# Kernel tuning notes

Measured on AMD Instinct MI355X. Metric: run time of the kernel, lower is better.

The kernel has to match this reference:

```python
import jax, jax.numpy as jnp
import numpy as np

D_MODEL = 1024
NUM_HEADS = 16
HEAD_DIM = D_MODEL // NUM_HEADS
BATCH = 2
SEQ = 2048
POS_DIM = 64


def setup_inputs() -> dict:
    key = jax.random.key(0)
    ks = jax.random.split(key, 6)
    s = 1.0 / np.sqrt(D_MODEL)
    return {
        "x": jax.random.normal(ks[0], (BATCH, SEQ, D_MODEL), jnp.float32),
        "positions": jax.random.normal(ks[1], (SEQ, POS_DIM), jnp.float32),
        "Wq": jax.random.normal(ks[2], (D_MODEL, D_MODEL), jnp.float32) * s,
        "bq": jnp.zeros((D_MODEL,), jnp.float32),
        "Wk": jax.random.normal(ks[3], (D_MODEL, D_MODEL), jnp.float32) * s,
        "bk": jnp.zeros((D_MODEL,), jnp.float32),
        "Wv": jax.random.normal(ks[4], (D_MODEL, D_MODEL), jnp.float32) * s,
        "bv": jnp.zeros((D_MODEL,), jnp.float32),
        "Wo": jax.random.normal(ks[5], (D_MODEL, D_MODEL), jnp.float32) * s,
        "bo": jnp.zeros((D_MODEL,), jnp.float32),
    }


def _geodesic_distances(positions):
    # Euclidean manifold: log_map(p_i, p_j) = p_j - p_i, metric = Identity
    # -> d(i,j) = ||p_j - p_i||_2 ; diagonal is exactly 0 (matches i!=j skip).
    diff = positions[None, :, :] - positions[:, None, :]  # [S, S, P]
    return jnp.sqrt(jnp.sum(diff * diff, axis=-1))        # [S, S]


def reference(x, positions, Wq, bq, Wk, bk, Wv, bv, Wo, bo):
    B, S, _ = x.shape
    q = (x @ Wq + bq).reshape(B, S, NUM_HEADS, HEAD_DIM)
    k = (x @ Wk + bk).reshape(B, S, NUM_HEADS, HEAD_DIM)
    v = (x @ Wv + bv).reshape(B, S, NUM_HEADS, HEAD_DIM)
    distances = _geodesic_distances(positions)  # [S, S]
    scores = jnp.einsum('bihd,bjhd->bhij', q, k) / jnp.sqrt(
        jnp.asarray(HEAD_DIM, x.dtype))
    scores = scores - distances[None, None, :, :]
    weights = jax.nn.softmax(scores, axis=-1)
    out = jnp.einsum('bhij,bjhd->bihd', weights, v).reshape(B, S, D_MODEL)
    return out @ Wo + bo
```

## Files before the change

kernel.cpp:

```cpp
#include <hip/hip_runtime.h>
#include <hip/hip_bf16.h>

typedef __attribute__((ext_vector_type(8))) short short8;
typedef __attribute__((ext_vector_type(4))) float f32x4;

#define S_LEN 2048
#define DM 1024
#define NH 16
#define HD 64
#define PD 64

#define LOG2E 1.4426950408889634f

#if __has_builtin(__builtin_amdgcn_exp2f)
#define EXP2F(x) __builtin_amdgcn_exp2f(x)
#else
#define EXP2F(x) exp2f(x)
#endif

#define WAIT4_BARRIER() do {                                   \
    asm volatile("s_waitcnt vmcnt(4)" ::: "memory");           \
    __builtin_amdgcn_sched_barrier(0);                         \
    __builtin_amdgcn_s_barrier();                              \
  } while (0)

static __device__ inline float bf2f(unsigned short u) {
  union { unsigned int i; float f; } c;
  c.i = ((unsigned int)u) << 16;
  return c.f;
}
static __device__ inline unsigned short f2bf(float f) {
  __hip_bfloat16 h = __float2bfloat16(f);
  return *reinterpret_cast<unsigned short*>(&h);
}

static __device__ __forceinline__ void glds16(const void* g, void* l) {
  __builtin_amdgcn_global_load_lds(
      (__attribute__((address_space(1))) unsigned int*)(unsigned long long)g,
      (__attribute__((address_space(3))) unsigned int*)l, 16, 0, 0);
}


__global__ void convx_kernel(const float* __restrict__ x,
                             __hip_bfloat16* __restrict__ xb, int n4) {
  int i = blockIdx.x * blockDim.x + threadIdx.x;
  if (i >= n4) return;
  const float4 v = reinterpret_cast<const float4*>(x)[i];
  union { __hip_bfloat16 h[4]; ushort4 u; } o;
  o.h[0] = __float2bfloat16(v.x);
  o.h[1] = __float2bfloat16(v.y);
  o.h[2] = __float2bfloat16(v.z);
  o.h[3] = __float2bfloat16(v.w);
  reinterpret_cast<ushort4*>(xb)[i] = o.u;
}

__global__ void posprep_kernel(const float* __restrict__ pos,
                               __hip_bfloat16* __restrict__ posb,
                               float* __restrict__ pnorm) {
  int row = blockIdx.x, c = threadIdx.x;
  float v = pos[row * PD + c];
  posb[row * PD + c] = __float2bfloat16(v);
  float s = v * v;
#pragma unroll
  for (int m = 1; m < 64; m <<= 1) s += __shfl_xor(s, m);
  if (c == 0) pnorm[row] = s;
}

__global__ __launch_bounds__(256) void wtrans_kernel(
    const float* __restrict__ W0, const float* __restrict__ W1,
    const float* __restrict__ W2, const float* __restrict__ W3,
    __hip_bfloat16* __restrict__ T0, __hip_bfloat16* __restrict__ T1,
    __hip_bfloat16* __restrict__ T2, __hip_bfloat16* __restrict__ T3) {
  __shared__ float tile[32][33];
  const float* W = blockIdx.z == 0 ? W0 : blockIdx.z == 1 ? W1
                 : blockIdx.z == 2 ? W2 : W3;
  __hip_bfloat16* T = blockIdx.z == 0 ? T0 : blockIdx.z == 1 ? T1
                    : blockIdx.z == 2 ? T2 : T3;
  int tx = threadIdx.x & 31, ty = threadIdx.x >> 5;
  int k0 = blockIdx.x * 32, n0 = blockIdx.y * 32;
#pragma unroll
  for (int q = 0; q < 4; ++q)
    tile[ty + q * 8][tx] = W[(size_t)(k0 + ty + q * 8) * DM + n0 + tx];
  __syncthreads();
#pragma unroll
  for (int q = 0; q < 4; ++q)
    T[(size_t)(n0 + ty + q * 8) * DM + k0 + tx] =
        __float2bfloat16(tile[tx][ty + q * 8]);
}

__global__ __launch_bounds__(256) void dmt_kernel(
    const __hip_bfloat16* __restrict__ posb, const float* __restrict__ pnorm,
    __hip_bfloat16* __restrict__ dtout) {
  int tid = threadIdx.x;
  int lane = tid & 63, wid = tid >> 6;
  int lr = lane & 15, lh = lane >> 4;
  int wr = wid >> 1, wc = wid & 1;
  int m0 = blockIdx.x * 128 + wr * 64;
  int n0 = blockIdx.y * 64 + wc * 32;

  f32x4 acc[4][2];
#pragma unroll
  for (int mi = 0; mi < 4; ++mi)
#pragma unroll
    for (int ni = 0; ni < 2; ++ni) acc[mi][ni] = (f32x4){0.f, 0.f, 0.f, 0.f};

  const __hip_bfloat16* Ap = posb + (size_t)(m0 + lr) * PD + lh * 8;
  const __hip_bfloat16* Bp = posb + (size_t)(n0 + lr) * PD + lh * 8;

#pragma unroll
  for (int k0 = 0; k0 < PD; k0 += 32) {
    short8 a[4], b[2];
#pragma unroll
    for (int mi = 0; mi < 4; ++mi)
      a[mi] = *reinterpret_cast<const short8*>(Ap + (size_t)mi * 16 * PD + k0);
#pragma unroll
    for (int ni = 0; ni < 2; ++ni)
      b[ni] = *reinterpret_cast<const short8*>(Bp + (size_t)ni * 16 * PD + k0);
#pragma unroll
    for (int mi = 0; mi < 4; ++mi)
#pragma unroll
      for (int ni = 0; ni < 2; ++ni)
        acc[mi][ni] = __builtin_amdgcn_mfma_f32_16x16x32_bf16(
            a[mi], b[ni], acc[mi][ni], 0, 0, 0);
  }

#pragma unroll
  for (int mi = 0; mi < 4; ++mi) {
    float nim[4];
#pragma unroll
    for (int r = 0; r < 4; ++r) nim[r] = pnorm[m0 + mi * 16 + lh * 4 + r];
#pragma unroll
    for (int ni = 0; ni < 2; ++ni) {
      int j = n0 + ni * 16 + lr;
      float nj = pnorm[j];
      ushort4 o;
      unsigned short* op = &o.x;
#pragma unroll
      for (int r = 0; r < 4; ++r) {
        int i = m0 + mi * 16 + lh * 4 + r;
        float d2 = nim[r] + nj - 2.f * acc[mi][ni][r];
        float dist = (i == j) ? 0.f : sqrtf(fmaxf(d2, 0.f));
        op[r] = f2bf(-dist * LOG2E);
      }
      int qt = (m0 + mi * 16) >> 4;
      *reinterpret_cast<ushort4*>(dtout + ((size_t)qt * S_LEN + j) * 16 + lh * 4) = o;
    }
  }
}

__global__ __launch_bounds__(256) void gemm_qkv_kernel(
    const __hip_bfloat16* __restrict__ A, const __hip_bfloat16* __restrict__ Bt,
    const float* __restrict__ bq, const float* __restrict__ bk,
    const float* __restrict__ bv, __hip_bfloat16* __restrict__ qb,
    __hip_bfloat16* __restrict__ kb, __hip_bfloat16* __restrict__ vt) {
  const int K = DM;
  __shared__ __hip_bfloat16 abuf[2][4096];
  __shared__ __hip_bfloat16 bbuf[2][4096];
  int tid = threadIdx.x;
  int lane = tid & 63, w = tid >> 6;
  int lr = lane & 15, lh = lane >> 4;
  int wr = w >> 1, wc = w & 1;
  int m0 = blockIdx.x * 128;
  int n0 = blockIdx.y * 128;

  f32x4 acc[4][4];
#pragma unroll
  for (int mi = 0; mi < 4; ++mi)
#pragma unroll
    for (int ni = 0; ni < 4; ++ni) acc[mi][ni] = (f32x4){0.f, 0.f, 0.f, 0.f};

  const __hip_bfloat16* Ag = A + (size_t)(m0 + lr) * K + lh * 8;
  const __hip_bfloat16* Bg = Bt + (size_t)(n0 + lr) * K + lh * 8;

  auto STAGE = [&](int nb, int k0) {
#pragma unroll
    for (int q = 0; q < 2; ++q) {
      int g = w * 2 + q;
      glds16(Ag + (size_t)(g * 16) * K + k0, &abuf[nb][g * 512]);
      glds16(Bg + (size_t)(g * 16) * K + k0, &bbuf[nb][g * 512]);
    }
  };

  STAGE(0, 0);

  const int NT = K / 32;
  for (int t = 0; t < NT; ++t) {
    int cb = t & 1;
    STAGE(cb ^ 1, (t + 1 < NT) ? (t + 1) * 32 : 0);
    WAIT4_BARRIER();
    short8 a[4], b[4];
#pragma unroll
    for (int mi = 0; mi < 4; ++mi)
      a[mi] = *reinterpret_cast<const short8*>(&abuf[cb][(wr * 4 + mi) * 512 + lane * 8]);
#pragma unroll
    for (int ni = 0; ni < 4; ++ni)
      b[ni] = *reinterpret_cast<const short8*>(&bbuf[cb][(wc * 4 + ni) * 512 + lane * 8]);
#pragma unroll
    for (int mi = 0; mi < 4; ++mi)
#pragma unroll
      for (int ni = 0; ni < 4; ++ni)
        acc[mi][ni] = __builtin_amdgcn_mfma_f32_16x16x32_bf16(
            a[mi], b[ni], acc[mi][ni], 0, 0, 0);
    __builtin_amdgcn_s_barrier();
  }

#pragma unroll
  for (int mi = 0; mi < 4; ++mi)
#pragma unroll
    for (int ni = 0; ni < 4; ++ni)
#pragma unroll
      for (int r = 0; r < 4; ++r) {
        int row = m0 + wr * 64 + mi * 16 + lh * 4 + r;
        int col = n0 + wc * 64 + ni * 16 + lr;
        int which = col >> 10, within = col & 1023;
        int bb = row >> 11, s = row & 2047;
        int h = within >> 6, d = within & 63;
        const float* bias = which == 0 ? bq : which == 1 ? bk : bv;
        float v = acc[mi][ni][r] + bias[within];
        __hip_bfloat16 hv = __float2bfloat16(v);
        if (which == 0)
          qb[((size_t)(bb * NH + h) * S_LEN + s) * HD + d] = hv;
        else if (which == 1)
          kb[((size_t)(bb * NH + h) * S_LEN + s) * HD + d] = hv;
        else
          vt[((size_t)(bb * NH + h) * HD + d) * S_LEN + s] = hv;
      }
}

__global__ __launch_bounds__(256) void gemm_out_kernel(
    const __hip_bfloat16* __restrict__ A, const __hip_bfloat16* __restrict__ Bt,
    const float* __restrict__ bias, float* __restrict__ out) {
  const int K = DM, N = DM;
  int tid = threadIdx.x;
  int lane = tid & 63, wid = tid >> 6;
  int lr = lane & 15, lh = lane >> 4;
  int wr = wid >> 1, wc = wid & 1;
  int m0 = blockIdx.x * 128 + wr * 64;
  int n0 = blockIdx.y * 64 + wc * 32;

  f32x4 acc[4][2];
#pragma unroll
  for (int mi = 0; mi < 4; ++mi)
#pragma unroll
    for (int ni = 0; ni < 2; ++ni) acc[mi][ni] = (f32x4){0.f, 0.f, 0.f, 0.f};

  const __hip_bfloat16* Ap = A + (size_t)(m0 + lr) * K + lh * 8;
  const __hip_bfloat16* Bp = Bt + (size_t)(n0 + lr) * K + lh * 8;

  for (int k0 = 0; k0 < K; k0 += 32) {
    short8 a[4], b[2];
#pragma unroll
    for (int mi = 0; mi < 4; ++mi)
      a[mi] = *reinterpret_cast<const short8*>(Ap + (size_t)mi * 16 * K + k0);
#pragma unroll
    for (int ni = 0; ni < 2; ++ni)
      b[ni] = *reinterpret_cast<const short8*>(Bp + (size_t)ni * 16 * K + k0);
#pragma unroll
    for (int mi = 0; mi < 4; ++mi)
#pragma unroll
      for (int ni = 0; ni < 2; ++ni)
        acc[mi][ni] = __builtin_amdgcn_mfma_f32_16x16x32_bf16(
            a[mi], b[ni], acc[mi][ni], 0, 0, 0);
  }

#pragma unroll
  for (int mi = 0; mi < 4; ++mi)
#pragma unroll
    for (int ni = 0; ni < 2; ++ni)
#pragma unroll
      for (int r = 0; r < 4; ++r) {
        int row = m0 + mi * 16 + lh * 4 + r;
        int col = n0 + ni * 16 + lr;
        out[(size_t)row * N + col] = acc[mi][ni][r] + bias[col];
      }
}

__global__ __launch_bounds__(256) void attn_kernel(
    const __hip_bfloat16* __restrict__ qb, const __hip_bfloat16* __restrict__ kb,
    const __hip_bfloat16* __restrict__ vt, const __hip_bfloat16* __restrict__ dt,
    __hip_bfloat16* __restrict__ ob) {
  __shared__ __hip_bfloat16 kbuf[2][4096];
  __shared__ __hip_bfloat16 vbuf[2][4096];
  __shared__ __hip_bfloat16 plds[4][16 * 64];
  int tid = threadIdx.x;
  int lane = tid & 63, w = tid >> 6;
  int lr = lane & 15, lh = lane >> 4;
  int bh = blockIdx.y;
  int b = bh >> 4, h = bh & 15;
  int s0 = blockIdx.x * 64 + w * 16;
  int qt = s0 >> 4;

  const __hip_bfloat16* qh = qb + (size_t)bh * S_LEN * HD;
  const __hip_bfloat16* kh = kb + (size_t)bh * S_LEN * HD;
  const __hip_bfloat16* vh = vt + (size_t)bh * HD * S_LEN;

  short8 qf0 = *reinterpret_cast<const short8*>(qh + (size_t)(s0 + lr) * HD + lh * 8);
  short8 qf1 = *reinterpret_cast<const short8*>(qh + (size_t)(s0 + lr) * HD + 32 + lh * 8);

  f32x4 accO[4];
#pragma unroll
  for (int n = 0; n < 4; ++n) accO[n] = (f32x4){0.f, 0.f, 0.f, 0.f};
  f32x4 lacc = (f32x4){0.f, 0.f, 0.f, 0.f};

  short8 ones;
#pragma unroll
  for (int e = 0; e < 8; ++e) ones[e] = (short)0x3F80;

  const f32x4 z4 = (f32x4){0.f, 0.f, 0.f, 0.f};
  const float C2 = 0.125f * LOG2E;

  const __hip_bfloat16* kstg = kh + (size_t)(w * 16 + lr) * HD + lh * 8;
  const __hip_bfloat16* vstg = vh + (size_t)(w * 16 + lr) * S_LEN + lh * 8;
  const __hip_bfloat16* dtq = dt + ((size_t)qt * S_LEN + lr) * 16 + lh * 4;

  auto STAGE = [&](int nb, int j0n) {
#pragma unroll
    for (int kk = 0; kk < 2; ++kk)
      glds16(kstg + (size_t)j0n * HD + kk * 32, &kbuf[nb][(w * 2 + kk) * 512]);
#pragma unroll
    for (int jj = 0; jj < 2; ++jj)
      glds16(vstg + j0n + jj * 32, &vbuf[nb][(w * 2 + jj) * 512]);
  };

  STAGE(0, 0);

  const int NT = S_LEN / 64;
  for (int t = 0; t < NT; ++t) {
    int cb = t & 1;
    int j0 = t * 64;

    ushort4 dv[4];
#pragma unroll
    for (int jt = 0; jt < 4; ++jt)
      dv[jt] = *reinterpret_cast<const ushort4*>(dtq + (size_t)(j0 + jt * 16) * 16);

    STAGE(cb ^ 1, (t + 1 < NT) ? j0 + 64 : 0);
    WAIT4_BARRIER();

#pragma unroll
    for (int jt = 0; jt < 4; ++jt) {
      short8 kf0 = *reinterpret_cast<const short8*>(&kbuf[cb][(jt * 2 + 0) * 512 + lane * 8]);
      short8 kf1 = *reinterpret_cast<const short8*>(&kbuf[cb][(jt * 2 + 1) * 512 + lane * 8]);
      f32x4 s4 = __builtin_amdgcn_mfma_f32_16x16x32_bf16(qf0, kf0, z4, 0, 0, 0);
      s4 = __builtin_amdgcn_mfma_f32_16x16x32_bf16(qf1, kf1, s4, 0, 0, 0);
      const unsigned short* dp = &dv[jt].x;
#pragma unroll
      for (int r = 0; r < 4; ++r) {
        float score2 = s4[r] * C2 + bf2f(dp[r]);
        float p = EXP2F(score2);
        int row = lh * 4 + r;
        int c = jt * 16 + lr;
        int idx = row * 64 + (((c >> 3) ^ (row & 7)) << 3) + (c & 7);
        plds[w][idx] = __float2bfloat16(p);
      }
    }
#pragma unroll
    for (int p2 = 0; p2 < 2; ++p2) {
      short8 pfrag = *reinterpret_cast<const short8*>(
          &plds[w][lr * 64 + ((((p2 * 4 + lh)) ^ (lr & 7)) << 3)]);
      lacc = __builtin_amdgcn_mfma_f32_16x16x32_bf16(pfrag, ones, lacc, 0, 0, 0);
#pragma unroll
      for (int n = 0; n < 4; ++n) {
        short8 vf = *reinterpret_cast<const short8*>(
            &vbuf[cb][(n * 2 + p2) * 512 + lane * 8]);
        accO[n] = __builtin_amdgcn_mfma_f32_16x16x32_bf16(pfrag, vf, accO[n], 0, 0, 0);
      }
    }
    __builtin_amdgcn_s_barrier();
  }

  float inv[4];
#pragma unroll
  for (int r = 0; r < 4; ++r) inv[r] = 1.f / lacc[r];
#pragma unroll
  for (int n = 0; n < 4; ++n)
#pragma unroll
    for (int r = 0; r < 4; ++r) {
      int s = s0 + lh * 4 + r;
      ob[((size_t)(b * S_LEN) + s) * DM + h * HD + n * 16 + lr] =
          __float2bfloat16(accO[n][r] * inv[r]);
    }
}

extern "C" void kernel_launch(void* const* d_in, const int* in_sizes, int n_in,
                              void* d_out, int out_size, void* d_ws, size_t ws_size,
                              hipStream_t stream) {
  const float* x   = (const float*)d_in[0];
  const float* pos = (const float*)d_in[1];
  const float* Wq  = (const float*)d_in[2];
  const float* bq  = (const float*)d_in[3];
  const float* Wk  = (const float*)d_in[4];
  const float* bk  = (const float*)d_in[5];
  const float* Wv  = (const float*)d_in[6];
  const float* bv  = (const float*)d_in[7];
  const float* Wo  = (const float*)d_in[8];
  const float* bo  = (const float*)d_in[9];

  char* ws = (char*)d_ws;
  size_t off = 0;
  auto alloc = [&](size_t bytes) {
    char* p = ws + off;
    off += (bytes + 255) & ~(size_t)255;
    return p;
  };
  __hip_bfloat16* xb    = (__hip_bfloat16*)alloc((size_t)4096 * DM * 2);
  __hip_bfloat16* wqkvT = (__hip_bfloat16*)alloc((size_t)3 * DM * DM * 2);
  __hip_bfloat16* woT   = (__hip_bfloat16*)alloc((size_t)DM * DM * 2);
  __hip_bfloat16* posb  = (__hip_bfloat16*)alloc((size_t)S_LEN * PD * 2);
  float*          pnrm  = (float*)alloc((size_t)S_LEN * 4);
  __hip_bfloat16* qb    = (__hip_bfloat16*)alloc((size_t)2 * NH * S_LEN * HD * 2);
  __hip_bfloat16* kb    = (__hip_bfloat16*)alloc((size_t)2 * NH * S_LEN * HD * 2);
  __hip_bfloat16* vt    = (__hip_bfloat16*)alloc((size_t)2 * NH * S_LEN * HD * 2);
  __hip_bfloat16* ob    = (__hip_bfloat16*)alloc((size_t)4096 * DM * 2);
  __hip_bfloat16* dtb   = (__hip_bfloat16*)alloc((size_t)(S_LEN / 16) * S_LEN * 16 * 2);
  (void)ws_size;

  int n4 = 4096 * DM / 4;
  hipLaunchKernelGGL(convx_kernel, dim3((n4 + 255) / 256), dim3(256), 0, stream,
                     x, xb, n4);
  hipLaunchKernelGGL(posprep_kernel, dim3(S_LEN), dim3(64), 0, stream,
                     pos, posb, pnrm);
  hipLaunchKernelGGL(wtrans_kernel, dim3(32, 32, 4), dim3(256), 0, stream,
                     Wq, Wk, Wv, Wo,
                     wqkvT, wqkvT + (size_t)DM * DM, wqkvT + (size_t)2 * DM * DM, woT);

  hipLaunchKernelGGL(dmt_kernel, dim3(S_LEN / 128, S_LEN / 64), dim3(256), 0, stream,
                     posb, pnrm, dtb);

  hipLaunchKernelGGL(gemm_qkv_kernel, dim3(4096 / 128, 3072 / 128), dim3(256), 0,
                     stream, xb, wqkvT, bq, bk, bv, qb, kb, vt);

  hipLaunchKernelGGL(attn_kernel, dim3(S_LEN / 64, 2 * NH), dim3(256), 0, stream,
                     qb, kb, vt, dtb, ob);

  hipLaunchKernelGGL(gemm_out_kernel, dim3(4096 / 128, DM / 64), dim3(256), 0,
                     stream, ob, woT, bo, (float*)d_out);
}
```

Before: 294.3 us.

## Keep softmax probabilities in registers via transposed QK MFMA feeding 16x16x16 PV MFMA

Swaps the operand order of the QK^T MFMA so each lane holds four consecutive key columns for one query row. Those probabilities then pack directly into a 16x16x16 bf16 MFMA A-operand, removing the per-warp LDS round trip for P and the ones-vector MFMA used to form row sums. Row sums are now kept in a scalar and combined with lane shuffles. The distance matrix producer is changed to a plain row-major layout to match the new access pattern. In exchange, the PV product uses twice as many smaller MFMAs and reads V with narrower LDS loads.

Measured after the change: 341.1 us. 15.9% more time.

```diff
diff --git a/kernel.cpp b/kernel.cpp
--- a/kernel.cpp
+++ b/kernel.cpp
@@ -2,6 +2,7 @@
 #include <hip/hip_bf16.h>
 
 typedef __attribute__((ext_vector_type(8))) short short8;
+typedef __attribute__((ext_vector_type(4))) short s16x4;
 typedef __attribute__((ext_vector_type(4))) float f32x4;
 
 #define S_LEN 2048
@@ -16,6 +17,20 @@
 #define EXP2F(x) __builtin_amdgcn_exp2f(x)
 #else
 #define EXP2F(x) exp2f(x)
+#endif
+
+#if __has_builtin(__builtin_amdgcn_mfma_f32_16x16x16bf16_1k)
+#define MFMA16(a, b, c) __builtin_amdgcn_mfma_f32_16x16x16bf16_1k((a), (b), (c), 0, 0, 0)
+#elif __has_builtin(__builtin_amdgcn_mfma_f32_16x16x16_bf16)
+#define MFMA16(a, b, c) __builtin_amdgcn_mfma_f32_16x16x16_bf16((a), (b), (c), 0, 0, 0)
+#else
+static __device__ __forceinline__ f32x4 mfma16_asm(s16x4 a, s16x4 b, f32x4 c) {
+  f32x4 d;
+  asm volatile("v_mfma_f32_16x16x16_bf16 %0, %1, %2, %3"
+               : "=v"(d) : "v"(a), "v"(b), "v"(c));
+  return d;
+}
+#define MFMA16(a, b, c) mfma16_asm((a), (b), (c))
 #endif
 
 #define WAIT4_BARRIER() do {                                   \
@@ -121,29 +136,28 @@
 #pragma unroll
       for (int ni = 0; ni < 2; ++ni)
         acc[mi][ni] = __builtin_amdgcn_mfma_f32_16x16x32_bf16(
-            a[mi], b[ni], acc[mi][ni], 0, 0, 0);
+            b[ni], a[mi], acc[mi][ni], 0, 0, 0);
   }
 
 #pragma unroll
   for (int mi = 0; mi < 4; ++mi) {
-    float nim[4];
-#pragma unroll
-    for (int r = 0; r < 4; ++r) nim[r] = pnorm[m0 + mi * 16 + lh * 4 + r];
+    int i = m0 + mi * 16 + lr;
+    float ni_ = pnorm[i];
 #pragma unroll
     for (int ni = 0; ni < 2; ++ni) {
-      int j = n0 + ni * 16 + lr;
-      float nj = pnorm[j];
+      int jb = n0 + ni * 16 + lh * 4;
+      float4 njv = *reinterpret_cast<const float4*>(pnorm + jb);
+      const float* njp = &njv.x;
       ushort4 o;
       unsigned short* op = &o.x;
 #pragma unroll
       for (int r = 0; r < 4; ++r) {
-        int i = m0 + mi * 16 + lh * 4 + r;
-        float d2 = nim[r] + nj - 2.f * acc[mi][ni][r];
+        int j = jb + r;
+        float d2 = ni_ + njp[r] - 2.f * acc[mi][ni][r];
         float dist = (i == j) ? 0.f : sqrtf(fmaxf(d2, 0.f));
         op[r] = f2bf(-dist * LOG2E);
       }
-      int qt = (m0 + mi * 16) >> 4;
-      *reinterpret_cast<ushort4*>(dtout + ((size_t)qt * S_LEN + j) * 16 + lh * 4) = o;
+      *reinterpret_cast<ushort4*>(dtout + (size_t)i * S_LEN + jb) = o;
     }
   }
 }
@@ -281,14 +295,12 @@
     __hip_bfloat16* __restrict__ ob) {
   __shared__ __hip_bfloat16 kbuf[2][4096];
   __shared__ __hip_bfloat16 vbuf[2][4096];
-  __shared__ __hip_bfloat16 plds[4][16 * 64];
   int tid = threadIdx.x;
   int lane = tid & 63, w = tid >> 6;
   int lr = lane & 15, lh = lane >> 4;
   int bh = blockIdx.y;
   int b = bh >> 4, h = bh & 15;
   int s0 = blockIdx.x * 64 + w * 16;
-  int qt = s0 >> 4;
 
   const __hip_bfloat16* qh = qb + (size_t)bh * S_LEN * HD;
   const __hip_bfloat16* kh = kb + (size_t)bh * S_LEN * HD;
@@ -300,18 +312,14 @@
   f32x4 accO[4];
 #pragma unroll
   for (int n = 0; n < 4; ++n) accO[n] = (f32x4){0.f, 0.f, 0.f, 0.f};
-  f32x4 lacc = (f32x4){0.f, 0.f, 0.f, 0.f};
-
-  short8 ones;
-#pragma unroll
-  for (int e = 0; e < 8; ++e) ones[e] = (short)0x3F80;
+  float lsum = 0.f;
 
   const f32x4 z4 = (f32x4){0.f, 0.f, 0.f, 0.f};
   const float C2 = 0.125f * LOG2E;
 
   const __hip_bfloat16* kstg = kh + (size_t)(w * 16 + lr) * HD + lh * 8;
   const __hip_bfloat16* vstg = vh + (size_t)(w * 16 + lr) * S_LEN + lh * 8;
-  const __hip_bfloat16* dtq = dt + ((size_t)qt * S_LEN + lr) * 16 + lh * 4;
+  const __hip_bfloat16* dtq = dt + (size_t)(s0 + lr) * S_LEN + lh * 4;
 
   auto STAGE = [&](int nb, int j0n) {
 #pragma unroll
@@ -323,6 +331,7 @@
   };
 
   STAGE(0, 0);
+
 
   const int NT = S_LEN / 64;
   for (int t = 0; t < NT; ++t) {
@@ -332,7 +341,7 @@
     ushort4 dv[4];
 #pragma unroll
     for (int jt = 0; jt < 4; ++jt)
-      dv[jt] = *reinterpret_cast<const ushort4*>(dtq + (size_t)(j0 + jt * 16) * 16);
+      dv[jt] = *reinterpret_cast<const ushort4*>(dtq + j0 + jt * 16);
 
     STAGE(cb ^ 1, (t + 1 < NT) ? j0 + 64 : 0);
     WAIT4_BARRIER();
@@ -341,44 +350,43 @@
     for (int jt = 0; jt < 4; ++jt) {
       short8 kf0 = *reinterpret_cast<const short8*>(&kbuf[cb][(jt * 2 + 0) * 512 + lane * 8]);
       short8 kf1 = *reinterpret_cast<const short8*>(&kbuf[cb][(jt * 2 + 1) * 512 + lane * 8]);
-      f32x4 s4 = __builtin_amdgcn_mfma_f32_16x16x32_bf16(qf0, kf0, z4, 0, 0, 0);
-      s4 = __builtin_amdgcn_mfma_f32_16x16x32_bf16(qf1, kf1, s4, 0, 0, 0);
+      f32x4 s4 = __builtin_amdgcn_mfma_f32_16x16x32_bf16(kf0, qf0, z4, 0, 0, 0);
+      s4 = __builtin_amdgcn_mfma_f32_16x16x32_bf16(kf1, qf1, s4, 0, 0, 0);
       const unsigned short* dp = &dv[jt].x;
-#pragma unroll
-      for (int r = 0; r < 4; ++r) {
-        float score2 = s4[r] * C2 + bf2f(dp[r]);
-        float p = EXP2F(score2);
-        int row = lh * 4 + r;
-        int c = jt * 16 + lr;
-        int idx = row * 64 + (((c >> 3) ^ (row & 7)) << 3) + (c & 7);
-        plds[w][idx] = __float2bfloat16(p);
-      }
-    }
-#pragma unroll
-    for (int p2 = 0; p2 < 2; ++p2) {
-      short8 pfrag = *reinterpret_cast<const short8*>(
-          &plds[w][lr * 64 + ((((p2 * 4 + lh)) ^ (lr & 7)) << 3)]);
-      lacc = __builtin_amdgcn_mfma_f32_16x16x32_bf16(pfrag, ones, lacc, 0, 0, 0);
+      float p[4];
+#pragma unroll
+      for (int r = 0; r < 4; ++r)
+        p[r] = EXP2F(s4[r] * C2 + bf2f(dp[r]));
+      lsum += (p[0] + p[1]) + (p[2] + p[3]);
+      union { s16x4 v; __hip_bfloat162 h2[2]; } up;
+      up.h2[0] = __float22bfloat162_rn(make_float2(p[0], p[1]));
+      up.h2[1] = __float22bfloat162_rn(make_float2(p[2], p[3]));
+      s16x4 pa = up.v;
+      int j64 = jt * 16 + lh * 4;
+      int voff = ((j64 >> 5) * 512) + (((j64 & 31) >> 3) * 16 + lr) * 8 + (j64 & 7);
 #pragma unroll
       for (int n = 0; n < 4; ++n) {
-        short8 vf = *reinterpret_cast<const short8*>(
-            &vbuf[cb][(n * 2 + p2) * 512 + lane * 8]);
-        accO[n] = __builtin_amdgcn_mfma_f32_16x16x32_bf16(pfrag, vf, accO[n], 0, 0, 0);
+        s16x4 vf = *reinterpret_cast<const s16x4*>(&vbuf[cb][n * 1024 + voff]);
+        accO[n] = MFMA16(pa, vf, accO[n]);
       }
     }
     __builtin_amdgcn_s_barrier();
   }
 
-  float inv[4];
-#pragma unroll
-  for (int r = 0; r < 4; ++r) inv[r] = 1.f / lacc[r];
+  lsum += __shfl_xor(lsum, 16);
+  lsum += __shfl_xor(lsum, 32);
+  float inv_ = 1.f / lsum;
+  float invr[4];
+#pragma unroll
+  for (int r = 0; r < 4; ++r) invr[r] = __shfl(inv_, lh * 4 + r);
+
 #pragma unroll
   for (int n = 0; n < 4; ++n)
 #pragma unroll
     for (int r = 0; r < 4; ++r) {
       int s = s0 + lh * 4 + r;
       ob[((size_t)(b * S_LEN) + s) * DM + h * HD + n * 16 + lr] =
-          __float2bfloat16(accO[n][r] * inv[r]);
+          __float2bfloat16(accO[n][r] * invr[r]);
     }
 }
 
@@ -412,7 +420,7 @@
   __hip_bfloat16* kb    = (__hip_bfloat16*)alloc((size_t)2 * NH * S_LEN * HD * 2);
   __hip_bfloat16* vt    = (__hip_bfloat16*)alloc((size_t)2 * NH * S_LEN * HD * 2);
   __hip_bfloat16* ob    = (__hip_bfloat16*)alloc((size_t)4096 * DM * 2);
-  __hip_bfloat16* dtb   = (__hip_bfloat16*)alloc((size_t)(S_LEN / 16) * S_LEN * 16 * 2);
+  __hip_bfloat16* dtb   = (__hip_bfloat16*)alloc((size_t)S_LEN * S_LEN * 2);
   (void)ws_size;
 
   int n4 = 4096 * DM / 4;
```

## Split attention KV range across two wave groups per block and merge partials

Applied to the files above, without the earlier changes.

The attention kernel now launches 512 threads per block. Two groups of four waves each process half of the key/value sequence, with 32-key tiles staged into separate LDS regions. At the end, the second half writes its unnormalized output accumulators and row sums to LDS, and the first half adds them before normalizing. This raises the number of waves per query tile to improve latency hiding and MFMA utilization. In exchange it adds a final LDS reduction and barrier, halves the tile size (more barriers per key), and leaves only two waves per group staging K and V.

After: 309.2 us. 5.1% more time.

```diff
diff --git a/kernel.cpp b/kernel.cpp
--- a/kernel.cpp
+++ b/kernel.cpp
@@ -275,25 +275,30 @@
       }
 }
 
-__global__ __launch_bounds__(256) void attn_kernel(
+__global__ __launch_bounds__(512, 8) void attn_kernel(
     const __hip_bfloat16* __restrict__ qb, const __hip_bfloat16* __restrict__ kb,
     const __hip_bfloat16* __restrict__ vt, const __hip_bfloat16* __restrict__ dt,
     __hip_bfloat16* __restrict__ ob) {
-  __shared__ __hip_bfloat16 kbuf[2][4096];
-  __shared__ __hip_bfloat16 vbuf[2][4096];
-  __shared__ __hip_bfloat16 plds[4][16 * 64];
+  __shared__ __align__(16) char smem[40960];
   int tid = threadIdx.x;
   int lane = tid & 63, w = tid >> 6;
+  int wq = w & 3, half = w >> 2;
   int lr = lane & 15, lh = lane >> 4;
   int bh = blockIdx.y;
   int b = bh >> 4, h = bh & 15;
-  int s0 = blockIdx.x * 64 + w * 16;
+  int s0 = blockIdx.x * 64 + wq * 16;
   int qt = s0 >> 4;
+  const int JH = S_LEN / 2;
+  int jbase = half * JH;
 
   const __hip_bfloat16* qh = qb + (size_t)bh * S_LEN * HD;
   const __hip_bfloat16* kh = kb + (size_t)bh * S_LEN * HD;
   const __hip_bfloat16* vh = vt + (size_t)bh * HD * S_LEN;
 
+  __hip_bfloat16* kbufB = (__hip_bfloat16*)(smem + half * 16384);
+  __hip_bfloat16* vbufB = (__hip_bfloat16*)(smem + half * 16384 + 8192);
+  __hip_bfloat16* pl    = (__hip_bfloat16*)(smem + 32768 + w * 1024);
+
   short8 qf0 = *reinterpret_cast<const short8*>(qh + (size_t)(s0 + lr) * HD + lh * 8);
   short8 qf1 = *reinterpret_cast<const short8*>(qh + (size_t)(s0 + lr) * HD + 32 + lh * 8);
 
@@ -309,77 +314,98 @@
   const f32x4 z4 = (f32x4){0.f, 0.f, 0.f, 0.f};
   const float C2 = 0.125f * LOG2E;
 
-  const __hip_bfloat16* kstg = kh + (size_t)(w * 16 + lr) * HD + lh * 8;
-  const __hip_bfloat16* vstg = vh + (size_t)(w * 16 + lr) * S_LEN + lh * 8;
   const __hip_bfloat16* dtq = dt + ((size_t)qt * S_LEN + lr) * 16 + lh * 4;
 
   auto STAGE = [&](int nb, int j0n) {
-#pragma unroll
-    for (int kk = 0; kk < 2; ++kk)
-      glds16(kstg + (size_t)j0n * HD + kk * 32, &kbuf[nb][(w * 2 + kk) * 512]);
-#pragma unroll
-    for (int jj = 0; jj < 2; ++jj)
-      glds16(vstg + j0n + jj * 32, &vbuf[nb][(w * 2 + jj) * 512]);
+    if (wq < 2) {
+#pragma unroll
+      for (int kk = 0; kk < 2; ++kk)
+        glds16(kh + (size_t)(j0n + wq * 16 + lr) * HD + kk * 32 + lh * 8,
+               kbufB + nb * 2048 + (wq * 2 + kk) * 512);
+    } else {
+      int w2 = wq - 2;
+#pragma unroll
+      for (int g = 0; g < 2; ++g)
+        glds16(vh + (size_t)((w2 * 2 + g) * 16 + lr) * S_LEN + j0n + lh * 8,
+               vbufB + nb * 2048 + (w2 * 2 + g) * 512);
+    }
   };
 
-  STAGE(0, 0);
-
-  const int NT = S_LEN / 64;
+  STAGE(0, jbase);
+
+  const int NT = JH / 32;
   for (int t = 0; t < NT; ++t) {
     int cb = t & 1;
-    int j0 = t * 64;
-
-    ushort4 dv[4];
-#pragma unroll
-    for (int jt = 0; jt < 4; ++jt)
+    int j0 = jbase + t * 32;
+
+    ushort4 dv[2];
+#pragma unroll
+    for (int jt = 0; jt < 2; ++jt)
       dv[jt] = *reinterpret_cast<const ushort4*>(dtq + (size_t)(j0 + jt * 16) * 16);
 
-    STAGE(cb ^ 1, (t + 1 < NT) ? j0 + 64 : 0);
+    STAGE(cb ^ 1, (t + 1 < NT) ? j0 + 32 : jbase);
     WAIT4_BARRIER();
 
 #pragma unroll
-    for (int jt = 0; jt < 4; ++jt) {
-      short8 kf0 = *reinterpret_cast<const short8*>(&kbuf[cb][(jt * 2 + 0) * 512 + lane * 8]);
-      short8 kf1 = *reinterpret_cast<const short8*>(&kbuf[cb][(jt * 2 + 1) * 512 + lane * 8]);
+    for (int jt = 0; jt < 2; ++jt) {
+      short8 kf0 = *reinterpret_cast<const short8*>(
+          kbufB + cb * 2048 + (jt * 2 + 0) * 512 + lane * 8);
+      short8 kf1 = *reinterpret_cast<const short8*>(
+          kbufB + cb * 2048 + (jt * 2 + 1) * 512 + lane * 8);
       f32x4 s4 = __builtin_amdgcn_mfma_f32_16x16x32_bf16(qf0, kf0, z4, 0, 0, 0);
       s4 = __builtin_amdgcn_mfma_f32_16x16x32_bf16(qf1, kf1, s4, 0, 0, 0);
       const unsigned short* dp = &dv[jt].x;
 #pragma unroll
       for (int r = 0; r < 4; ++r) {
-        float score2 = s4[r] * C2 + bf2f(dp[r]);
-        float p = EXP2F(score2);
+        float p = EXP2F(s4[r] * C2 + bf2f(dp[r]));
         int row = lh * 4 + r;
         int c = jt * 16 + lr;
-        int idx = row * 64 + (((c >> 3) ^ (row & 7)) << 3) + (c & 7);
-        plds[w][idx] = __float2bfloat16(p);
+        int idx = row * 32 + ((((c >> 3) ^ ((row >> 1) & 3))) << 3) + (c & 7);
+        pl[idx] = __float2bfloat16(p);
       }
     }
-#pragma unroll
-    for (int p2 = 0; p2 < 2; ++p2) {
-      short8 pfrag = *reinterpret_cast<const short8*>(
-          &plds[w][lr * 64 + ((((p2 * 4 + lh)) ^ (lr & 7)) << 3)]);
-      lacc = __builtin_amdgcn_mfma_f32_16x16x32_bf16(pfrag, ones, lacc, 0, 0, 0);
-#pragma unroll
-      for (int n = 0; n < 4; ++n) {
-        short8 vf = *reinterpret_cast<const short8*>(
-            &vbuf[cb][(n * 2 + p2) * 512 + lane * 8]);
-        accO[n] = __builtin_amdgcn_mfma_f32_16x16x32_bf16(pfrag, vf, accO[n], 0, 0, 0);
-      }
+    short8 pfrag = *reinterpret_cast<const short8*>(
+        pl + lr * 32 + ((lh ^ ((lr >> 1) & 3)) << 3));
+    lacc = __builtin_amdgcn_mfma_f32_16x16x32_bf16(pfrag, ones, lacc, 0, 0, 0);
+#pragma unroll
+    for (int n = 0; n < 4; ++n) {
+      short8 vf = *reinterpret_cast<const short8*>(
+          vbufB + cb * 2048 + n * 512 + lane * 8);
+      accO[n] = __builtin_amdgcn_mfma_f32_16x16x32_bf16(pfrag, vf, accO[n], 0, 0, 0);
     }
     __builtin_amdgcn_s_barrier();
   }
 
-  float inv[4];
-#pragma unroll
-  for (int r = 0; r < 4; ++r) inv[r] = 1.f / lacc[r];
-#pragma unroll
-  for (int n = 0; n < 4; ++n)
-#pragma unroll
-    for (int r = 0; r < 4; ++r) {
-      int s = s0 + lh * 4 + r;
-      ob[((size_t)(b * S_LEN) + s) * DM + h * HD + n * 16 + lr] =
-          __float2bfloat16(accO[n][r] * inv[r]);
-    }
+  asm volatile("s_waitcnt vmcnt(0)" ::: "memory");
+  __builtin_amdgcn_s_barrier();
+
+  float* mb = (float*)smem;
+  if (half == 1) {
+    float* dst = mb + (size_t)(wq * 64 + lane) * 20;
+#pragma unroll
+    for (int n = 0; n < 4; ++n)
+      *reinterpret_cast<f32x4*>(dst + n * 4) = accO[n];
+    *reinterpret_cast<f32x4*>(dst + 16) = lacc;
+  }
+  __syncthreads();
+  if (half == 0) {
+    const float* src = mb + (size_t)(wq * 64 + lane) * 20;
+#pragma unroll
+    for (int n = 0; n < 4; ++n)
+      accO[n] += *reinterpret_cast<const f32x4*>(src + n * 4);
+    lacc += *reinterpret_cast<const f32x4*>(src + 16);
+    float inv[4];
+#pragma unroll
+    for (int r = 0; r < 4; ++r) inv[r] = 1.f / lacc[r];
+#pragma unroll
+    for (int n = 0; n < 4; ++n)
+#pragma unroll
+      for (int r = 0; r < 4; ++r) {
+        int s = s0 + lh * 4 + r;
+        ob[((size_t)(b * S_LEN) + s) * DM + h * HD + n * 16 + lr] =
+            __float2bfloat16(accO[n][r] * inv[r]);
+      }
+  }
 }
 
 extern "C" void kernel_launch(void* const* d_in, const int* in_sizes, int n_in,
@@ -430,7 +456,7 @@
   hipLaunchKernelGGL(gemm_qkv_kernel, dim3(4096 / 128, 3072 / 128), dim3(256), 0,
                      stream, xb, wqkvT, bq, bk, bv, qb, kb, vt);
 
-  hipLaunchKernelGGL(attn_kernel, dim3(S_LEN / 64, 2 * NH), dim3(256), 0, stream,
+  hipLaunchKernelGGL(attn_kernel, dim3(S_LEN / 64, 2 * NH), dim3(512), 0, stream,
                      qb, kb, vt, dtb, ob);
 
   hipLaunchKernelGGL(gemm_out_kernel, dim3(4096 / 128, DM / 64), dim3(256), 0,
```
